# Optimization experiments

Hardware: AMD Instinct MI355X
Metric: run time of the kernel (lower is better)

The kernel has to match this reference:

```python
import jax, jax.numpy as jnp
import numpy as np

N_NODES = 100000
N_EDGES = 1600000
IN_CH = 64
HID = 64
N_GRAPHS = 64


def _sage_conv(x, src, dst, Wl, bl, Wr, n_nodes):
    # PyG SAGEConv (aggr='mean'): out = lin_l(mean_{j in N(i)} x_j) + lin_r(x_i)
    msg = x[src]                                            # [E, d] gather
    agg = jax.ops.segment_sum(msg, dst, num_segments=n_nodes)
    cnt = jax.ops.segment_sum(jnp.ones((src.shape[0],), x.dtype), dst,
                              num_segments=n_nodes)
    agg = agg / jnp.maximum(cnt, 1.0)[:, None]
    return agg @ Wl + bl + x @ Wr


def setup_inputs() -> dict:
    key = jax.random.key(0)
    ks = jax.random.split(key, 16)
    x = jax.random.normal(ks[0], (N_NODES, IN_CH), jnp.float32)
    edge_index = jax.random.randint(ks[1], (2, N_EDGES), 0, N_NODES, jnp.int64)
    batch = jnp.sort(jax.random.randint(ks[2], (N_NODES,), 0, N_GRAPHS, jnp.int64))

    def glorot(k, fan_in, fan_out):
        s = jnp.sqrt(2.0 / (fan_in + fan_out))
        return jax.random.normal(k, (fan_in, fan_out), jnp.float32) * s

    params = {
        'W1l': glorot(ks[3], IN_CH, HID), 'b1': jnp.zeros((HID,), jnp.float32),
        'W1r': glorot(ks[4], IN_CH, HID),
        'W2l': glorot(ks[5], HID, HID), 'b2': jnp.zeros((HID,), jnp.float32),
        'W2r': glorot(ks[6], HID, HID),
        'W3l': glorot(ks[7], HID, HID), 'b3': jnp.zeros((HID,), jnp.float32),
        'W3r': glorot(ks[8], HID, HID),
        'Wc1': glorot(ks[9], HID, HID // 2), 'bc1': jnp.zeros((HID // 2,), jnp.float32),
        'Wc2': glorot(ks[10], HID // 2, 2), 'bc2': jnp.zeros((2,), jnp.float32),
    }
    return {'x': x, 'edge_index': edge_index, 'batch': batch, **params}


def reference(x, edge_index, batch,
              W1l, b1, W1r, W2l, b2, W2r, W3l, b3, W3r,
              Wc1, bc1, Wc2, bc2):
    src, dst = edge_index[0], edge_index[1]
    n = x.shape[0]
    h = jax.nn.relu(_sage_conv(x, src, dst, W1l, b1, W1r, n))   # dropout = identity (eval)
    h = jax.nn.relu(_sage_conv(h, src, dst, W2l, b2, W2r, n))
    h = jax.nn.relu(_sage_conv(h, src, dst, W3l, b3, W3r, n))
    # global mean pool over graphs
    sums = jax.ops.segment_sum(h, batch, num_segments=N_GRAPHS)
    cnts = jax.ops.segment_sum(jnp.ones((n,), h.dtype), batch, num_segments=N_GRAPHS)
    g = sums / jnp.maximum(cnts, 1.0)[:, None]                  # [G, HID]
    # MLP head (dropout = identity at eval)
    return jax.nn.relu(g @ Wc1 + bc1) @ Wc2 + bc2               # [G, 2]
```

## Files before the change

### kernel.cpp

```cpp
#include <hip/hip_runtime.h>
#include <hip/hip_bf16.h>
#include <hip/hip_fp16.h>

typedef unsigned int u32;
typedef unsigned short u16;
typedef _Float16 f16x8 __attribute__((ext_vector_type(8)));
typedef float f32x4 __attribute__((ext_vector_type(4)));

#define NBLK1 512
#define CVTBLK 256

__device__ __forceinline__ u16 f2h(float f) { return __half_as_ushort(__float2half(f)); }
__device__ __forceinline__ u32 packh2(float a, float b) {
    return (u32)f2h(a) | ((u32)f2h(b) << 16);
}

__device__ __forceinline__ int gidx(const void* p, long long i, int w64) {
    if (w64) return (int)((const long long*)p)[i];
    return ((const int*)p)[i];
}

__device__ __forceinline__ int detect_w64(const int* edge_words, int E, int tid, int* sh) {
    if (tid == 0) *sh = 0;
    __syncthreads();
    const long long totalWords = 2LL * E;
    const long long step = totalWords / 256;
    long long w = ((long long)tid * step) | 1;
    int nz = (w < totalWords) ? edge_words[w] : 0;
    if (nz) atomicOr(sh, 1);
    __syncthreads();
    return (*sh) ? 0 : 1;
}

__global__ void __launch_bounds__(256) fused_hist_cvt(
        const void* __restrict__ edge, int* __restrict__ flag, u32* __restrict__ ticket,
        u32* __restrict__ HG, int E, int n, int nb1,
        const float* __restrict__ X, u16* __restrict__ Xh) {
    if (blockIdx.x < NBLK1) {
        __shared__ u32 h[256];
        __shared__ int shnz;
        const int tid = threadIdx.x;
        h[tid] = 0;
        const int w64 = detect_w64((const int*)edge, E, tid, &shnz);
        if (blockIdx.x == 0 && tid == 0) { flag[0] = w64; ticket[0] = 0; }
        __syncthreads();
        const int chunk = (E + NBLK1 - 1) / NBLK1;
        const int s = blockIdx.x * chunk;
        const int e = min(s + chunk, E);
        for (int i = s + tid; i < e; i += 256) {
            int d = gidx(edge, (long long)E + i, w64);
            if ((unsigned)d >= (unsigned)n) d = 0;
            atomicAdd(&h[d >> 9], 1);
        }
        __syncthreads();
        for (int b = tid; b < nb1; b += 256) HG[b * NBLK1 + blockIdx.x] = h[b];
        return;
    }
    const long long total4 = (long long)n * 16;
    const long long stride = (long long)CVTBLK * 256;
    long long i = (long long)(blockIdx.x - NBLK1) * 256 + threadIdx.x;
    const float4* X4 = (const float4*)X;
    uint2* O = (uint2*)Xh;
    for (; i < total4; i += stride) {
        float4 v = X4[i];
        uint2 o;
        o.x = packh2(v.x, v.y);
        o.y = packh2(v.z, v.w);
        O[i] = o;
    }
}

__global__ void scanAB(u32* __restrict__ HG, u32* __restrict__ blockSums,
                       u32* __restrict__ SB, u32* __restrict__ ticket, int n) {
    __shared__ u32 ts[256];
    __shared__ int isLast;
    const int ITEMS = 8;
    const int tid = threadIdx.x;
    int base = blockIdx.x * 2048 + tid * ITEMS;
    u32 v[ITEMS];
    u32 sum = 0;
#pragma unroll
    for (int i = 0; i < ITEMS; ++i) {
        int idx = base + i;
        v[i] = (idx < n) ? HG[idx] : 0;
        sum += v[i];
    }
    ts[tid] = sum;
    __syncthreads();
    u32 incl = sum;
    for (int d = 1; d < 256; d <<= 1) {
        u32 y = 0;
        if (tid >= d) y = ts[tid - d];
        __syncthreads();
        incl += y;
        ts[tid] = incl;
        __syncthreads();
    }
    u32 run = incl - sum;
#pragma unroll
    for (int i = 0; i < ITEMS; ++i) {
        int idx = base + i;
        if (idx < n) HG[idx] = run;
        run += v[i];
    }
    if (tid == 255) {
        atomicExch(&blockSums[blockIdx.x], incl);
        __threadfence();
        u32 t = atomicAdd(&ticket[0], 1u);
        isLast = (t == gridDim.x - 1);
    }
    __syncthreads();
    if (!isLast) return;
    const int nb = gridDim.x;
    u32 bv = (tid < nb) ? atomicAdd(&blockSums[tid], 0u) : 0;
    ts[tid] = bv;
    __syncthreads();
    u32 bincl = bv;
    for (int d = 1; d < 256; d <<= 1) {
        u32 y = 0;
        if (tid >= d) y = ts[tid - d];
        __syncthreads();
        bincl += y;
        ts[tid] = bincl;
        __syncthreads();
    }
    if (tid < nb) SB[tid] = bincl - bv;
}

__global__ void __launch_bounds__(256) p1_scatter(const void* __restrict__ edge,
                                                  const int* __restrict__ flag,
                                                  const u32* __restrict__ HG,
                                                  const u32* __restrict__ SB,
                                                  u32* __restrict__ P, int E, int n, int nb1) {
    __shared__ u32 base[256];
    __shared__ u32 cur[256];
    const int tid = threadIdx.x;
    cur[tid] = 0;
    for (int b = tid; b < nb1; b += 256) {
        int i = b * NBLK1 + blockIdx.x;
        base[b] = HG[i] + SB[i >> 11];
    }
    __syncthreads();
    const int w64 = flag[0];
    const int chunk = (E + NBLK1 - 1) / NBLK1;
    const int s = blockIdx.x * chunk;
    const int e = min(s + chunk, E);
    for (int i = s + tid; i < e; i += 256) {
        int d = gidx(edge, (long long)E + i, w64);
        if ((unsigned)d >= (unsigned)n) d = 0;
        int sv = gidx(edge, i, w64);
        if ((unsigned)sv >= (unsigned)n) sv = 0;
        const int b1 = d >> 9;
        u32 r = atomicAdd(&cur[b1], 1);
        P[base[b1] + r] = (u32)sv | ((u32)(d & 511) << 17);
    }
}

__global__ void __launch_bounds__(512) p2_kernel(const u32* __restrict__ P,
                                                 const u32* __restrict__ HG,
                                                 const u32* __restrict__ SB,
                                                 u32* __restrict__ offs,
                                                 int* __restrict__ ss,
                                                 float* __restrict__ pool,
                                                 int E, int n, int nb1) {
    __shared__ u32 h2[512];
    __shared__ u32 ts[512];
    const int tid = threadIdx.x;
    const int b = blockIdx.x;
    if (b == 0)
        for (int i = tid; i < 4096; i += 512) pool[i] = 0.f;
    const int i0 = b * NBLK1;
    const int bs = (int)(HG[i0] + SB[i0 >> 11]);
    int be;
    if (b + 1 < nb1) {
        const int i1 = (b + 1) * NBLK1;
        be = (int)(HG[i1] + SB[i1 >> 11]);
    } else be = E;
    h2[tid] = 0;
    __syncthreads();
    for (int i = bs + tid; i < be; i += 512) atomicAdd(&h2[(P[i] >> 17) & 511], 1);
    __syncthreads();
    u32 v = h2[tid];
    ts[tid] = v;
    __syncthreads();
    u32 incl = v;
    for (int d = 1; d < 512; d <<= 1) {
        u32 y = 0;
        if (tid >= d) y = ts[tid - d];
        __syncthreads();
        incl += y;
        ts[tid] = incl;
        __syncthreads();
    }
    u32 run = incl - v;
    h2[tid] = run;
    const int node0 = b * 512 + tid;
    if (node0 < n) offs[node0] = bs + run;
    if (b == 0 && tid == 0) offs[n] = (u32)E;
    __syncthreads();
    for (int i = bs + tid; i < be; i += 512) {
        u32 p = P[i];
        u32 r = atomicAdd(&h2[(p >> 17) & 511], 1);
        ss[bs + r] = (int)(p & 0x1FFFFu);
    }
}

__global__ void __launch_bounds__(256) sage_layer(
        const u16* __restrict__ G, const u32* __restrict__ offs,
        const int* __restrict__ ss,
        const float* __restrict__ Wl, const float* __restrict__ Wr,
        const float* __restrict__ Bv,
        u16* __restrict__ Hout, float* __restrict__ pool,
        const void* __restrict__ batch, const int* __restrict__ flag,
        int n, int mode) {
    const int lane = threadIdx.x & 63;
    const int quad = lane >> 4;
    const int m16 = lane & 15;
    f16x8 bl[2][4], br[2][4];
#pragma unroll
    for (int kh = 0; kh < 2; ++kh)
#pragma unroll
        for (int t = 0; t < 4; ++t)
#pragma unroll
            for (int j = 0; j < 8; ++j) {
                int k = kh * 32 + quad * 8 + j;
                int c = t * 16 + m16;
                bl[kh][t][j] = (_Float16)Wl[k * 64 + c];
                br[kh][t][j] = (_Float16)Wr[k * 64 + c];
            }
    float bias_t[4];
#pragma unroll
    for (int t = 0; t < 4; ++t) bias_t[t] = Bv[t * 16 + m16];
    const int w64 = mode ? flag[0] : 0;

    const int ntiles = (n + 15) >> 4;
    const int nwaves = gridDim.x * 4;
    for (int tile = blockIdx.x * 4 + (threadIdx.x >> 6); tile < ntiles; tile += nwaves) {
        const int nodeBase = tile << 4;
        const int node_m = nodeBase + m16;
        const int nodeA = node_m < n ? node_m : n - 1;
        const u32 o0 = offs[nodeA];
        const u32 o1 = offs[nodeA + 1];
        const int deg = node_m < n ? (int)(o1 - o0) : 0;
        f16x8 s0, s1;
#pragma unroll
        for (int j = 0; j < 8; ++j) { s0[j] = (_Float16)0; s1[j] = (_Float16)0; }
        int e = 0;
        for (; e + 2 <= deg; e += 2) {
            const int sA = ss[o0 + e];
            const int sB = ss[o0 + e + 1];
            const f16x8* pa = (const f16x8*)(G + ((size_t)sA << 6)) + quad;
            const f16x8* pb = (const f16x8*)(G + ((size_t)sB << 6)) + quad;
            f16x8 a0 = pa[0], a1 = pa[4];
            f16x8 b0 = pb[0], b1 = pb[4];
            s0 += a0; s1 += a1;
            s0 += b0; s1 += b1;
        }
        if (e < deg) {
            const int sA = ss[o0 + e];
            const f16x8* pa = (const f16x8*)(G + ((size_t)sA << 6)) + quad;
            s0 += pa[0]; s1 += pa[4];
        }
        const float rdf = deg > 0 ? 1.f / (float)deg : 0.f;
        const _Float16 hrd = (_Float16)rdf;
#pragma unroll
        for (int j = 0; j < 8; ++j) { s0[j] *= hrd; s1[j] *= hrd; }
        const f16x8 as0 = *(const f16x8*)(G + (size_t)nodeA * 64 + quad * 8);
        const f16x8 as1 = *(const f16x8*)(G + (size_t)nodeA * 64 + 32 + quad * 8);
        f32x4 c[4];
#pragma unroll
        for (int t = 0; t < 4; ++t) {
            f32x4 acc = {bias_t[t], bias_t[t], bias_t[t], bias_t[t]};
            acc = __builtin_amdgcn_mfma_f32_16x16x32_f16(s0, bl[0][t], acc, 0, 0, 0);
            acc = __builtin_amdgcn_mfma_f32_16x16x32_f16(s1, bl[1][t], acc, 0, 0, 0);
            acc = __builtin_amdgcn_mfma_f32_16x16x32_f16(as0, br[0][t], acc, 0, 0, 0);
            acc = __builtin_amdgcn_mfma_f32_16x16x32_f16(as1, br[1][t], acc, 0, 0, 0);
            c[t] = acc;
        }
        if (mode == 0) {
#pragma unroll
            for (int rg = 0; rg < 4; ++rg) {
                const int node = nodeBase + quad * 4 + rg;
                if (node < n) {
#pragma unroll
                    for (int t = 0; t < 4; ++t)
                        Hout[(size_t)node * 64 + t * 16 + m16] = f2h(fmaxf(c[t][rg], 0.f));
                }
            }
        } else {
            float v[4][4];
#pragma unroll
            for (int t = 0; t < 4; ++t)
#pragma unroll
                for (int rg = 0; rg < 4; ++rg) v[t][rg] = fmaxf(c[t][rg], 0.f);
            const int lastN = nodeBase + 15 < n ? nodeBase + 15 : n - 1;
            const int g0 = gidx(batch, nodeBase, w64) & 63;
            const int g1 = gidx(batch, lastN, w64) & 63;
            if (nodeBase + 15 < n && g0 == g1) {
#pragma unroll
                for (int t = 0; t < 4; ++t) {
                    float cs = v[t][0] + v[t][1] + v[t][2] + v[t][3];
                    cs += __shfl_xor(cs, 16, 64);
                    cs += __shfl_xor(cs, 32, 64);
                    if (quad == 0) atomicAdd(&pool[g0 * 64 + t * 16 + m16], cs);
                }
            } else {
#pragma unroll
                for (int rg = 0; rg < 4; ++rg) {
                    const int node = nodeBase + quad * 4 + rg;
                    if (node < n) {
                        const int g = gidx(batch, node, w64) & 63;
#pragma unroll
                        for (int t = 0; t < 4; ++t)
                            atomicAdd(&pool[g * 64 + t * 16 + m16], v[t][rg]);
                    }
                }
            }
        }
    }
}

__global__ void head_kernel(const float* __restrict__ pool, const void* __restrict__ batch,
                            const int* __restrict__ flag,
                            const float* __restrict__ Wc1, const float* __restrict__ bc1,
                            const float* __restrict__ Wc2, const float* __restrict__ bc2,
                            float* __restrict__ out, int n) {
    __shared__ float gm[64 * 64];
    __shared__ float am[64 * 32];
    __shared__ int cnts[64];
    const int tid = threadIdx.x;
    const int w64 = flag[0];
    if (tid < 64) {
        int lo = 0, hi = n;
        while (lo < hi) { int mid = (lo + hi) >> 1; if (gidx(batch, mid, w64) < tid) lo = mid + 1; else hi = mid; }
        int lo2 = 0, hi2 = n;
        int v2 = tid + 1;
        while (lo2 < hi2) { int mid = (lo2 + hi2) >> 1; if (gidx(batch, mid, w64) < v2) lo2 = mid + 1; else hi2 = mid; }
        cnts[tid] = lo2 - lo;
    }
    __syncthreads();
    for (int i = tid; i < 4096; i += 256) {
        int g = i >> 6;
        float c = (float)(cnts[g] > 0 ? cnts[g] : 1);
        gm[i] = pool[i] / c;
    }
    __syncthreads();
    for (int i = tid; i < 64 * 32; i += 256) {
        int g = i >> 5, j = i & 31;
        float acc = bc1[j];
        for (int k = 0; k < 64; ++k) acc += gm[g * 64 + k] * Wc1[k * 32 + j];
        am[i] = acc > 0.f ? acc : 0.f;
    }
    __syncthreads();
    if (tid < 128) {
        int g = tid >> 1, o = tid & 1;
        float acc = bc2[o];
        for (int j = 0; j < 32; ++j) acc += am[g * 32 + j] * Wc2[j * 2 + o];
        out[tid] = acc;
    }
}

extern "C" void kernel_launch(void* const* d_in, const int* in_sizes, int n_in,
                              void* d_out, int out_size, void* d_ws, size_t ws_size,
                              hipStream_t stream) {
    const float* x   = (const float*)d_in[0];
    const void* edge = d_in[1];
    const void* batch = d_in[2];
    const float* W1l = (const float*)d_in[3];
    const float* b1  = (const float*)d_in[4];
    const float* W1r = (const float*)d_in[5];
    const float* W2l = (const float*)d_in[6];
    const float* b2  = (const float*)d_in[7];
    const float* W2r = (const float*)d_in[8];
    const float* W3l = (const float*)d_in[9];
    const float* b3  = (const float*)d_in[10];
    const float* W3r = (const float*)d_in[11];
    const float* Wc1 = (const float*)d_in[12];
    const float* bc1 = (const float*)d_in[13];
    const float* Wc2 = (const float*)d_in[14];
    const float* bc2 = (const float*)d_in[15];

    const int n = in_sizes[0] / 64;
    const int E = in_sizes[1] / 2;
    const int nb1 = (n + 511) >> 9;
    const int NS = nb1 * NBLK1;

    char* w = (char*)d_ws;
    size_t o = 0;
    auto take = [&](size_t bytes) -> void* {
        void* p = w + o;
        o = (o + bytes + 511) & ~(size_t)511;
        return p;
    };
    int* flag      = (int*)take(sizeof(int));
    u32* ticket    = (u32*)take(2 * sizeof(u32));
    u32* offs      = (u32*)take((size_t)(n + 1) * sizeof(u32));
    u32* HG        = (u32*)take((size_t)(NS + 1) * sizeof(u32));
    u32* blockSums = (u32*)take(256 * sizeof(u32));
    u32* SB        = (u32*)take(256 * sizeof(u32));
    u32* P         = (u32*)take((size_t)E * sizeof(u32));
    int* ss        = (int*)take((size_t)E * sizeof(int));
    u16* Xh        = (u16*)take((size_t)n * 64 * sizeof(u16));
    u16* HA        = (u16*)take((size_t)n * 64 * sizeof(u16));
    u16* HB        = (u16*)take((size_t)n * 64 * sizeof(u16));
    float* pool    = (float*)take(64 * 64 * sizeof(float));

    fused_hist_cvt<<<NBLK1 + CVTBLK, 256, 0, stream>>>(edge, flag, ticket, HG, E, n, nb1,
                                                       x, Xh);
    const int nbScan = (NS + 2047) / 2048;
    scanAB<<<nbScan, 256, 0, stream>>>(HG, blockSums, SB, ticket, NS);
    p1_scatter<<<NBLK1, 256, 0, stream>>>(edge, flag, HG, SB, P, E, n, nb1);
    p2_kernel<<<nb1, 512, 0, stream>>>(P, HG, SB, offs, ss, pool, E, n, nb1);

    const int ntiles = (n + 15) >> 4;
    const int SLBLK = (ntiles + 3) >> 2;
    sage_layer<<<SLBLK, 256, 0, stream>>>(Xh, offs, ss, W1l, W1r, b1, HA, nullptr,
                                          batch, flag, n, 0);
    sage_layer<<<SLBLK, 256, 0, stream>>>(HA, offs, ss, W2l, W2r, b2, HB, nullptr,
                                          batch, flag, n, 0);
    sage_layer<<<SLBLK, 256, 0, stream>>>(HB, offs, ss, W3l, W3r, b3, nullptr, pool,
                                          batch, flag, n, 1);
    head_kernel<<<1, 256, 0, stream>>>(pool, batch, flag, Wc1, bc1, Wc2, bc2,
                                       (float*)d_out, n);
}
```

Baseline: 306.3 us.

## Split SAGE layer into separate aggregation and MFMA matmul kernels

Each SAGE layer is split into two kernels. The first does only the mean-neighbor gather, unrolled 4 edges deep, with launch bounds allowing 8 blocks per CU, and writes the result to a new fp16 buffer M. The second, launched on a fixed 256-block grid, loads M and the self features and runs the MFMA weight products, so weight loading is amortized over fewer blocks. This is meant to free the gather from the weight-fragment registers and raise occupancy and memory parallelism. In exchange it adds an extra write and read of an n×64 fp16 buffer plus three more kernel launches.

```diff
diff --git a/kernel.cpp b/kernel.cpp
--- a/kernel.cpp
+++ b/kernel.cpp
@@ -9,6 +9,7 @@
 
 #define NBLK1 512
 #define CVTBLK 256
+#define MMBLK 256
 
 __device__ __forceinline__ u16 f2h(float f) { return __half_as_ushort(__float2half(f)); }
 __device__ __forceinline__ u32 packh2(float a, float b) {
@@ -205,9 +206,59 @@
     }
 }
 
-__global__ void __launch_bounds__(256) sage_layer(
+__global__ void __launch_bounds__(256, 8) agg_kernel(
         const u16* __restrict__ G, const u32* __restrict__ offs,
-        const int* __restrict__ ss,
+        const int* __restrict__ ss, u16* __restrict__ M, int n) {
+    const int lane = threadIdx.x & 63;
+    const int quad = lane >> 4;
+    const int m16 = lane & 15;
+    const int ntiles = (n + 15) >> 4;
+    const int nwaves = gridDim.x * 4;
+    for (int tile = blockIdx.x * 4 + (threadIdx.x >> 6); tile < ntiles; tile += nwaves) {
+        const int nodeBase = tile << 4;
+        const int node_m = nodeBase + m16;
+        const int valid = node_m < n;
+        const int nodeA = valid ? node_m : n - 1;
+        const u32 o0 = offs[nodeA];
+        const int deg = valid ? (int)(offs[nodeA + 1] - o0) : 0;
+        const int* sp = ss + o0;
+        f16x8 s0, s1;
+#pragma unroll
+        for (int j = 0; j < 8; ++j) { s0[j] = (_Float16)0; s1[j] = (_Float16)0; }
+        int e = 0;
+        for (; e + 4 <= deg; e += 4) {
+            const int iA = sp[e], iB = sp[e + 1], iC = sp[e + 2], iD = sp[e + 3];
+            const f16x8* pA = (const f16x8*)(G + ((size_t)iA << 6)) + quad;
+            const f16x8* pB = (const f16x8*)(G + ((size_t)iB << 6)) + quad;
+            const f16x8* pC = (const f16x8*)(G + ((size_t)iC << 6)) + quad;
+            const f16x8* pD = (const f16x8*)(G + ((size_t)iD << 6)) + quad;
+            f16x8 a0 = pA[0], a1 = pA[4];
+            f16x8 b0 = pB[0], b1 = pB[4];
+            f16x8 c0 = pC[0], c1 = pC[4];
+            f16x8 d0 = pD[0], d1 = pD[4];
+            s0 += a0; s1 += a1;
+            s0 += b0; s1 += b1;
+            s0 += c0; s1 += c1;
+            s0 += d0; s1 += d1;
+        }
+        for (; e < deg; ++e) {
+            const int iA = sp[e];
+            const f16x8* pA = (const f16x8*)(G + ((size_t)iA << 6)) + quad;
+            s0 += pA[0]; s1 += pA[4];
+        }
+        const float rdf = deg > 0 ? 1.f / (float)deg : 0.f;
+        const _Float16 hrd = (_Float16)rdf;
+#pragma unroll
+        for (int j = 0; j < 8; ++j) { s0[j] *= hrd; s1[j] *= hrd; }
+        if (valid) {
+            *(f16x8*)(M + (size_t)node_m * 64 + quad * 8) = s0;
+            *(f16x8*)(M + (size_t)node_m * 64 + 32 + quad * 8) = s1;
+        }
+    }
+}
+
+__global__ void __launch_bounds__(256) mm_fused(
+        const u16* __restrict__ M, const u16* __restrict__ G,
         const float* __restrict__ Wl, const float* __restrict__ Wr,
         const float* __restrict__ Bv,
         u16* __restrict__ Hout, float* __restrict__ pool,
@@ -239,40 +290,16 @@
         const int nodeBase = tile << 4;
         const int node_m = nodeBase + m16;
         const int nodeA = node_m < n ? node_m : n - 1;
-        const u32 o0 = offs[nodeA];
-        const u32 o1 = offs[nodeA + 1];
-        const int deg = node_m < n ? (int)(o1 - o0) : 0;
-        f16x8 s0, s1;
-#pragma unroll
-        for (int j = 0; j < 8; ++j) { s0[j] = (_Float16)0; s1[j] = (_Float16)0; }
-        int e = 0;
-        for (; e + 2 <= deg; e += 2) {
-            const int sA = ss[o0 + e];
-            const int sB = ss[o0 + e + 1];
-            const f16x8* pa = (const f16x8*)(G + ((size_t)sA << 6)) + quad;
-            const f16x8* pb = (const f16x8*)(G + ((size_t)sB << 6)) + quad;
-            f16x8 a0 = pa[0], a1 = pa[4];
-            f16x8 b0 = pb[0], b1 = pb[4];
-            s0 += a0; s1 += a1;
-            s0 += b0; s1 += b1;
-        }
-        if (e < deg) {
-            const int sA = ss[o0 + e];
-            const f16x8* pa = (const f16x8*)(G + ((size_t)sA << 6)) + quad;
-            s0 += pa[0]; s1 += pa[4];
-        }
-        const float rdf = deg > 0 ? 1.f / (float)deg : 0.f;
-        const _Float16 hrd = (_Float16)rdf;
-#pragma unroll
-        for (int j = 0; j < 8; ++j) { s0[j] *= hrd; s1[j] *= hrd; }
+        const f16x8 am0 = *(const f16x8*)(M + (size_t)nodeA * 64 + quad * 8);
+        const f16x8 am1 = *(const f16x8*)(M + (size_t)nodeA * 64 + 32 + quad * 8);
         const f16x8 as0 = *(const f16x8*)(G + (size_t)nodeA * 64 + quad * 8);
         const f16x8 as1 = *(const f16x8*)(G + (size_t)nodeA * 64 + 32 + quad * 8);
         f32x4 c[4];
 #pragma unroll
         for (int t = 0; t < 4; ++t) {
             f32x4 acc = {bias_t[t], bias_t[t], bias_t[t], bias_t[t]};
-            acc = __builtin_amdgcn_mfma_f32_16x16x32_f16(s0, bl[0][t], acc, 0, 0, 0);
-            acc = __builtin_amdgcn_mfma_f32_16x16x32_f16(s1, bl[1][t], acc, 0, 0, 0);
+            acc = __builtin_amdgcn_mfma_f32_16x16x32_f16(am0, bl[0][t], acc, 0, 0, 0);
+            acc = __builtin_amdgcn_mfma_f32_16x16x32_f16(am1, bl[1][t], acc, 0, 0, 0);
             acc = __builtin_amdgcn_mfma_f32_16x16x32_f16(as0, br[0][t], acc, 0, 0, 0);
             acc = __builtin_amdgcn_mfma_f32_16x16x32_f16(as1, br[1][t], acc, 0, 0, 0);
             c[t] = acc;
@@ -403,6 +430,7 @@
     u16* Xh        = (u16*)take((size_t)n * 64 * sizeof(u16));
     u16* HA        = (u16*)take((size_t)n * 64 * sizeof(u16));
     u16* HB        = (u16*)take((size_t)n * 64 * sizeof(u16));
+    u16* M         = (u16*)take((size_t)n * 64 * sizeof(u16));
     float* pool    = (float*)take(64 * 64 * sizeof(float));
 
     fused_hist_cvt<<<NBLK1 + CVTBLK, 256, 0, stream>>>(edge, flag, ticket, HG, E, n, nb1,
@@ -413,13 +441,14 @@
     p2_kernel<<<nb1, 512, 0, stream>>>(P, HG, SB, offs, ss, pool, E, n, nb1);
 
     const int ntiles = (n + 15) >> 4;
-    const int SLBLK = (ntiles + 3) >> 2;
-    sage_layer<<<SLBLK, 256, 0, stream>>>(Xh, offs, ss, W1l, W1r, b1, HA, nullptr,
-                                          batch, flag, n, 0);
-    sage_layer<<<SLBLK, 256, 0, stream>>>(HA, offs, ss, W2l, W2r, b2, HB, nullptr,
-                                          batch, flag, n, 0);
-    sage_layer<<<SLBLK, 256, 0, stream>>>(HB, offs, ss, W3l, W3r, b3, nullptr, pool,
-                                          batch, flag, n, 1);
+    const int AGGBLK = (ntiles + 3) >> 2;
+    agg_kernel<<<AGGBLK, 256, 0, stream>>>(Xh, offs, ss, M, n);
+    mm_fused<<<MMBLK, 256, 0, stream>>>(M, Xh, W1l, W1r, b1, HA, nullptr, batch, flag, n, 0);
+    agg_kernel<<<AGGBLK, 256, 0, stream>>>(HA, offs, ss, M, n);
+    mm_fused<<<MMBLK, 256, 0, stream>>>(M, HA, W2l, W2r, b2, HB, nullptr, batch, flag, n, 0);
+    agg_kernel<<<AGGBLK, 256, 0, stream>>>(HB, offs, ss, M, n);
+    mm_fused<<<MMBLK, 256, 0, stream>>>(M, HB, W3l, W3r, b3, nullptr, pool, batch, flag, n, 1);
+
     head_kernel<<<1, 256, 0, stream>>>(pool, batch, flag, Wc1, bc1, Wc2, bc2,
                                        (float*)d_out, n);
 }
```

New measurement: 302.1 us. Within noise of the previous version (-1.4%).

## Stage SAGE weights in LDS, unroll neighbor gather by four, raise occupancy

Applied to the files above, without the earlier changes.

Each SAGE layer block now converts and stores both 64x64 weight matrices in shared memory in an MFMA-friendly swizzled order, instead of holding 16 f16x8 weight fragments per lane in registers. Fragments are read from LDS per output tile. The neighbor gather loop is unrolled from 2 to 4 edges to put more loads in flight, and launch bounds ask for 8 waves-per-EU occupancy. This trades register pressure and latency for LDS reads and 16 KB of shared memory per block, and with about 1563 small blocks every block repeats the weight staging plus a barrier.

```diff
diff --git a/kernel.cpp b/kernel.cpp
--- a/kernel.cpp
+++ b/kernel.cpp
@@ -205,7 +205,7 @@
     }
 }
 
-__global__ void __launch_bounds__(256) sage_layer(
+__global__ void __launch_bounds__(256, 8) sage2(
         const u16* __restrict__ G, const u32* __restrict__ offs,
         const int* __restrict__ ss,
         const float* __restrict__ Wl, const float* __restrict__ Wr,
@@ -213,53 +213,58 @@
         u16* __restrict__ Hout, float* __restrict__ pool,
         const void* __restrict__ batch, const int* __restrict__ flag,
         int n, int mode) {
-    const int lane = threadIdx.x & 63;
+    __shared__ _Float16 WlS[4096];
+    __shared__ _Float16 WrS[4096];
+    __shared__ float BS[64];
+    const int tid = threadIdx.x;
+    for (int idx = tid; idx < 4096; idx += 256) {
+        const int k = idx >> 6, c = idx & 63;
+        const int dst = ((((k >> 5) * 4 + ((k >> 3) & 3)) * 4 + (c >> 4)) * 16 + (c & 15)) * 8
+                        + (k & 7);
+        WlS[dst] = (_Float16)Wl[idx];
+        WrS[dst] = (_Float16)Wr[idx];
+    }
+    if (tid < 64) BS[tid] = Bv[tid];
+    __syncthreads();
+
+    const int lane = tid & 63;
     const int quad = lane >> 4;
     const int m16 = lane & 15;
-    f16x8 bl[2][4], br[2][4];
-#pragma unroll
-    for (int kh = 0; kh < 2; ++kh)
-#pragma unroll
-        for (int t = 0; t < 4; ++t)
-#pragma unroll
-            for (int j = 0; j < 8; ++j) {
-                int k = kh * 32 + quad * 8 + j;
-                int c = t * 16 + m16;
-                bl[kh][t][j] = (_Float16)Wl[k * 64 + c];
-                br[kh][t][j] = (_Float16)Wr[k * 64 + c];
-            }
-    float bias_t[4];
-#pragma unroll
-    for (int t = 0; t < 4; ++t) bias_t[t] = Bv[t * 16 + m16];
     const int w64 = mode ? flag[0] : 0;
+    const _Float16* wlp = WlS + (quad * 4 * 16 + m16) * 8;
+    const _Float16* wrp = WrS + (quad * 4 * 16 + m16) * 8;
 
     const int ntiles = (n + 15) >> 4;
     const int nwaves = gridDim.x * 4;
-    for (int tile = blockIdx.x * 4 + (threadIdx.x >> 6); tile < ntiles; tile += nwaves) {
+    for (int tile = blockIdx.x * 4 + (tid >> 6); tile < ntiles; tile += nwaves) {
         const int nodeBase = tile << 4;
         const int node_m = nodeBase + m16;
         const int nodeA = node_m < n ? node_m : n - 1;
         const u32 o0 = offs[nodeA];
-        const u32 o1 = offs[nodeA + 1];
-        const int deg = node_m < n ? (int)(o1 - o0) : 0;
+        const int deg = node_m < n ? (int)(offs[nodeA + 1] - o0) : 0;
+        const int* sp = ss + o0;
         f16x8 s0, s1;
 #pragma unroll
         for (int j = 0; j < 8; ++j) { s0[j] = (_Float16)0; s1[j] = (_Float16)0; }
         int e = 0;
-        for (; e + 2 <= deg; e += 2) {
-            const int sA = ss[o0 + e];
-            const int sB = ss[o0 + e + 1];
-            const f16x8* pa = (const f16x8*)(G + ((size_t)sA << 6)) + quad;
-            const f16x8* pb = (const f16x8*)(G + ((size_t)sB << 6)) + quad;
-            f16x8 a0 = pa[0], a1 = pa[4];
-            f16x8 b0 = pb[0], b1 = pb[4];
+        for (; e + 4 <= deg; e += 4) {
+            const int iA = sp[e], iB = sp[e + 1], iC = sp[e + 2], iD = sp[e + 3];
+            const f16x8* pA = (const f16x8*)(G + ((size_t)iA << 6)) + quad;
+            const f16x8* pB = (const f16x8*)(G + ((size_t)iB << 6)) + quad;
+            const f16x8* pC = (const f16x8*)(G + ((size_t)iC << 6)) + quad;
+            const f16x8* pD = (const f16x8*)(G + ((size_t)iD << 6)) + quad;
+            f16x8 a0 = pA[0], a1 = pA[4];
+            f16x8 b0 = pB[0], b1 = pB[4];
+            f16x8 c0 = pC[0], c1 = pC[4];
+            f16x8 d0 = pD[0], d1 = pD[4];
             s0 += a0; s1 += a1;
             s0 += b0; s1 += b1;
+            s0 += c0; s1 += c1;
+            s0 += d0; s1 += d1;
         }
-        if (e < deg) {
-            const int sA = ss[o0 + e];
-            const f16x8* pa = (const f16x8*)(G + ((size_t)sA << 6)) + quad;
-            s0 += pa[0]; s1 += pa[4];
+        for (; e < deg; ++e) {
+            const f16x8* pA = (const f16x8*)(G + ((size_t)(sp[e]) << 6)) + quad;
+            s0 += pA[0]; s1 += pA[4];
         }
         const float rdf = deg > 0 ? 1.f / (float)deg : 0.f;
         const _Float16 hrd = (_Float16)rdf;
@@ -267,52 +272,45 @@
         for (int j = 0; j < 8; ++j) { s0[j] *= hrd; s1[j] *= hrd; }
         const f16x8 as0 = *(const f16x8*)(G + (size_t)nodeA * 64 + quad * 8);
         const f16x8 as1 = *(const f16x8*)(G + (size_t)nodeA * 64 + 32 + quad * 8);
-        f32x4 c[4];
 #pragma unroll
         for (int t = 0; t < 4; ++t) {
-            f32x4 acc = {bias_t[t], bias_t[t], bias_t[t], bias_t[t]};
-            acc = __builtin_amdgcn_mfma_f32_16x16x32_f16(s0, bl[0][t], acc, 0, 0, 0);
-            acc = __builtin_amdgcn_mfma_f32_16x16x32_f16(s1, bl[1][t], acc, 0, 0, 0);
-            acc = __builtin_amdgcn_mfma_f32_16x16x32_f16(as0, br[0][t], acc, 0, 0, 0);
-            acc = __builtin_amdgcn_mfma_f32_16x16x32_f16(as1, br[1][t], acc, 0, 0, 0);
-            c[t] = acc;
-        }
-        if (mode == 0) {
-#pragma unroll
-            for (int rg = 0; rg < 4; ++rg) {
-                const int node = nodeBase + quad * 4 + rg;
-                if (node < n) {
-#pragma unroll
-                    for (int t = 0; t < 4; ++t)
-                        Hout[(size_t)node * 64 + t * 16 + m16] = f2h(fmaxf(c[t][rg], 0.f));
+            const float bt = BS[t * 16 + m16];
+            const f16x8 l0 = *(const f16x8*)(wlp + t * 128);
+            const f16x8 l1 = *(const f16x8*)(wlp + 2048 + t * 128);
+            const f16x8 r0 = *(const f16x8*)(wrp + t * 128);
+            const f16x8 r1 = *(const f16x8*)(wrp + 2048 + t * 128);
+            f32x4 acc = {bt, bt, bt, bt};
+            acc = __builtin_amdgcn_mfma_f32_16x16x32_f16(s0, l0, acc, 0, 0, 0);
+            acc = __builtin_amdgcn_mfma_f32_16x16x32_f16(s1, l1, acc, 0, 0, 0);
+            acc = __builtin_amdgcn_mfma_f32_16x16x32_f16(as0, r0, acc, 0, 0, 0);
+            acc = __builtin_amdgcn_mfma_f32_16x16x32_f16(as1, r1, acc, 0, 0, 0);
+            if (mode == 0) {
+#pragma unroll
+                for (int rg = 0; rg < 4; ++rg) {
+                    const int node = nodeBase + quad * 4 + rg;
+                    if (node < n)
+                        Hout[(size_t)node * 64 + t * 16 + m16] = f2h(fmaxf(acc[rg], 0.f));
                 }
-            }
-        } else {
-            float v[4][4];
-#pragma unroll
-            for (int t = 0; t < 4; ++t)
-#pragma unroll
-                for (int rg = 0; rg < 4; ++rg) v[t][rg] = fmaxf(c[t][rg], 0.f);
-            const int lastN = nodeBase + 15 < n ? nodeBase + 15 : n - 1;
-            const int g0 = gidx(batch, nodeBase, w64) & 63;
-            const int g1 = gidx(batch, lastN, w64) & 63;
-            if (nodeBase + 15 < n && g0 == g1) {
-#pragma unroll
-                for (int t = 0; t < 4; ++t) {
-                    float cs = v[t][0] + v[t][1] + v[t][2] + v[t][3];
+            } else {
+                float v0 = fmaxf(acc[0], 0.f), v1 = fmaxf(acc[1], 0.f);
+                float v2 = fmaxf(acc[2], 0.f), v3 = fmaxf(acc[3], 0.f);
+                const int lastN = nodeBase + 15 < n ? nodeBase + 15 : n - 1;
+                const int g0 = gidx(batch, nodeBase, w64) & 63;
+                const int g1 = gidx(batch, lastN, w64) & 63;
+                if (nodeBase + 15 < n && g0 == g1) {
+                    float cs = v0 + v1 + v2 + v3;
                     cs += __shfl_xor(cs, 16, 64);
                     cs += __shfl_xor(cs, 32, 64);
                     if (quad == 0) atomicAdd(&pool[g0 * 64 + t * 16 + m16], cs);
-                }
-            } else {
-#pragma unroll
-                for (int rg = 0; rg < 4; ++rg) {
-                    const int node = nodeBase + quad * 4 + rg;
-                    if (node < n) {
-                        const int g = gidx(batch, node, w64) & 63;
-#pragma unroll
-                        for (int t = 0; t < 4; ++t)
-                            atomicAdd(&pool[g * 64 + t * 16 + m16], v[t][rg]);
+                } else {
+                    const float vv[4] = {v0, v1, v2, v3};
+#pragma unroll
+                    for (int rg = 0; rg < 4; ++rg) {
+                        const int node = nodeBase + quad * 4 + rg;
+                        if (node < n) {
+                            const int g = gidx(batch, node, w64) & 63;
+                            atomicAdd(&pool[g * 64 + t * 16 + m16], vv[rg]);
+                        }
                     }
                 }
             }
@@ -414,12 +412,12 @@
 
     const int ntiles = (n + 15) >> 4;
     const int SLBLK = (ntiles + 3) >> 2;
-    sage_layer<<<SLBLK, 256, 0, stream>>>(Xh, offs, ss, W1l, W1r, b1, HA, nullptr,
-                                          batch, flag, n, 0);
-    sage_layer<<<SLBLK, 256, 0, stream>>>(HA, offs, ss, W2l, W2r, b2, HB, nullptr,
-                                          batch, flag, n, 0);
-    sage_layer<<<SLBLK, 256, 0, stream>>>(HB, offs, ss, W3l, W3r, b3, nullptr, pool,
-                                          batch, flag, n, 1);
+    sage2<<<SLBLK, 256, 0, stream>>>(Xh, offs, ss, W1l, W1r, b1, HA, nullptr,
+                                     batch, flag, n, 0);
+    sage2<<<SLBLK, 256, 0, stream>>>(HA, offs, ss, W2l, W2r, b2, HB, nullptr,
+                                     batch, flag, n, 0);
+    sage2<<<SLBLK, 256, 0, stream>>>(HB, offs, ss, W3l, W3r, b3, nullptr, pool,
+                                     batch, flag, n, 1);
     head_kernel<<<1, 256, 0, stream>>>(pool, batch, flag, Wc1, bc1, Wc2, bc2,
                                        (float*)d_out, n);
 }
```

New measurement: 408.4 us. 33.3% more time.
